# Kernel tuning notes

Hardware: AMD Instinct MI355X
Metric: run time of the kernel (lower is better)

The kernel has to match this reference:

```python
import jax, jax.numpy as jnp
import numpy as np

DIM = 2048
NUM_HEADS = 16
HEAD_DIM = DIM // NUM_HEADS  # 128
B, T = 2, 2048
ROPE_BASE = 10000.0


def _rope_tables(seq_len, head_dim, dtype=jnp.float32):
    inv_freq = 1.0 / (ROPE_BASE ** (jnp.arange(0, head_dim, 2, dtype=jnp.float32) / head_dim))
    t = jnp.arange(seq_len, dtype=jnp.float32)
    freqs = jnp.einsum('i,j->ij', t, inv_freq)          # [T, head_dim/2]
    emb = jnp.concatenate([freqs, freqs], axis=-1)       # [T, head_dim]
    return jnp.cos(emb).astype(dtype), jnp.sin(emb).astype(dtype)


def _rotate_half(x):
    x1, x2 = jnp.split(x, 2, axis=-1)
    return jnp.concatenate([-x2, x1], axis=-1)


def setup_inputs() -> dict:
    key = jax.random.key(0)
    k1, k2, k3 = jax.random.split(key, 3)
    x = jax.random.normal(k1, (B, T, DIM), dtype=jnp.float32)
    w_qkv = jax.random.normal(k2, (3 * DIM, DIM), dtype=jnp.float32) * (DIM ** -0.5)
    w_out = jax.random.normal(k3, (DIM, DIM), dtype=jnp.float32) * (DIM ** -0.5)
    return {"x": x, "w_qkv": w_qkv, "w_out": w_out}


def reference(x, w_qkv, w_out):
    b, t, _ = x.shape
    scale = HEAD_DIM ** -0.5

    qkv = x @ w_qkv.T                                    # [B, T, 3*dim]
    q, k, v = jnp.split(qkv, 3, axis=-1)
    # [B, H, T, hd]
    q = q.reshape(b, t, NUM_HEADS, HEAD_DIM).transpose(0, 2, 1, 3)
    k = k.reshape(b, t, NUM_HEADS, HEAD_DIM).transpose(0, 2, 1, 3)
    v = v.reshape(b, t, NUM_HEADS, HEAD_DIM).transpose(0, 2, 1, 3)

    cos, sin = _rope_tables(t, HEAD_DIM, x.dtype)        # [T, hd] broadcast over B,H
    q = q * cos + _rotate_half(q) * sin
    k = k * cos + _rotate_half(k) * sin

    scores = jnp.einsum('bhqd,bhkd->bhqk', q, k) * scale  # [B, H, T, T]
    causal = jnp.tril(jnp.ones((t, t), dtype=bool))
    scores = jnp.where(causal, scores, jnp.float32(-jnp.inf).astype(scores.dtype))
    attn = jax.nn.softmax(scores, axis=-1)
    out = jnp.einsum('bhqk,bhkd->bhqd', attn, v)         # [B, H, T, hd]
    out = out.transpose(0, 2, 1, 3).reshape(b, t, DIM)
    out = out @ w_out.T
    return out
```

## Files before the change

kernel.cpp:

```cpp
#include <hip/hip_runtime.h>
#include <hip/hip_bf16.h>
#include <stdint.h>
#include <math.h>

#define DIMC 2048
#define NH 16
#define HD 128
#define BBATCH 2
#define TSEQ 2048
#define MROWS (BBATCH*TSEQ)
#define NQKV (3*DIMC)

typedef __attribute__((ext_vector_type(8))) short short8;
typedef __attribute__((ext_vector_type(4))) float f32x4;

__device__ __forceinline__ short f2bf(float f) {
  union { float f; uint32_t u; } v; v.f = f;
  uint32_t r = (v.u + 0x7fffu + ((v.u >> 16) & 1u)) >> 16;
  return (short)(uint16_t)r;
}
__device__ __forceinline__ float bf2f(short s) {
  union { uint32_t u; float f; } v; v.u = ((uint32_t)(uint16_t)s) << 16;
  return v.f;
}
__device__ __forceinline__ void g2lds16(const void* g, void* l) {
  __builtin_amdgcn_global_load_lds((const __attribute__((address_space(1))) void*)g,
                                   (__attribute__((address_space(3))) void*)l, 16, 0, 0);
}

__global__ void rope_tables(float* __restrict__ cos_t, float* __restrict__ sin_t) {
  int idx = blockIdx.x * blockDim.x + threadIdx.x;
  int t = idx >> 6, j = idx & 63;
  double inv = exp(-((double)(2 * j) / 128.0) * log(10000.0));
  float fr = (float)t * (float)inv;
  cos_t[idx] = cosf(fr);
  sin_t[idx] = sinf(fr);
}

__global__ void cast_f32_bf16(const float* __restrict__ in, short* __restrict__ out, int n8) {
  int i = blockIdx.x * blockDim.x + threadIdx.x;
  if (i >= n8) return;
  const float4* p = (const float4*)in;
  float4 a = p[2 * i], b = p[2 * i + 1];
  short8 o;
  o[0] = f2bf(a.x); o[1] = f2bf(a.y); o[2] = f2bf(a.z); o[3] = f2bf(a.w);
  o[4] = f2bf(b.x); o[5] = f2bf(b.y); o[6] = f2bf(b.z); o[7] = f2bf(b.w);
  ((short8*)out)[i] = o;
}

__global__ void rope_apply(short* __restrict__ q, short* __restrict__ k,
                           const float* __restrict__ cos_t, const float* __restrict__ sin_t) {
  int idx = blockIdx.x * blockDim.x + threadIdx.x;
  int j = idx & 63;
  int t = (idx >> 6) & (TSEQ - 1);
  int bh = idx >> 17;
  size_t base = ((size_t)bh * TSEQ + t) * HD;
  float c = cos_t[t * 64 + j], s = sin_t[t * 64 + j];
  float x1 = bf2f(q[base + j]), x2 = bf2f(q[base + j + 64]);
  q[base + j]      = f2bf(x1 * c - x2 * s);
  q[base + j + 64] = f2bf(x2 * c + x1 * s);
  float y1 = bf2f(k[base + j]), y2 = bf2f(k[base + j + 64]);
  k[base + j]      = f2bf(y1 * c - y2 * s);
  k[base + j + 64] = f2bf(y2 * c + y1 * s);
}

template<int EPI>
__global__ __launch_bounds__(256)
void gemm_bt(const short* __restrict__ A, const short* __restrict__ B,
             int M, int N, int K,
             float* __restrict__ Cout,
             short* __restrict__ qp, short* __restrict__ kp, short* __restrict__ vp) {
  __shared__ short As[128 * 32];
  __shared__ short Bs[128 * 32];
  int tid = threadIdx.x;
  int lane = tid & 63, wave = tid >> 6;
  int wr = wave >> 1, wc = wave & 1;
  int bm = blockIdx.y, bn = blockIdx.x;
  int rowA0 = bm * 128, rowB0 = bn * 128;
  f32x4 acc[4][4] = {};
  for (int k0 = 0; k0 < K; k0 += 32) {
    #pragma unroll
    for (int j = 0; j < 2; ++j) {
      int c = tid + j * 256;
      int r = c >> 2, kk = (c & 3) * 8;
      g2lds16(A + (size_t)(rowA0 + r) * K + k0 + kk, As + c * 8);
      g2lds16(B + (size_t)(rowB0 + r) * K + k0 + kk, Bs + c * 8);
    }
    __syncthreads();
    short8 af[4], bfr[4];
    #pragma unroll
    for (int mf = 0; mf < 4; ++mf)
      af[mf] = *(const short8*)(As + (wr * 64 + mf * 16 + (lane & 15)) * 32 + 8 * (lane >> 4));
    #pragma unroll
    for (int nf = 0; nf < 4; ++nf)
      bfr[nf] = *(const short8*)(Bs + (wc * 64 + nf * 16 + (lane & 15)) * 32 + 8 * (lane >> 4));
    #pragma unroll
    for (int mf = 0; mf < 4; ++mf)
      #pragma unroll
      for (int nf = 0; nf < 4; ++nf)
        acc[mf][nf] = __builtin_amdgcn_mfma_f32_16x16x32_bf16(af[mf], bfr[nf], acc[mf][nf], 0, 0, 0);
    __syncthreads();
  }
  if (EPI == 1) {
    #pragma unroll
    for (int mf = 0; mf < 4; ++mf)
      #pragma unroll
      for (int nf = 0; nf < 4; ++nf)
        #pragma unroll
        for (int i = 0; i < 4; ++i) {
          int gm = rowA0 + wr * 64 + mf * 16 + ((lane >> 4) << 2) + i;
          int gn = rowB0 + wc * 64 + nf * 16 + (lane & 15);
          Cout[(size_t)gm * N + gn] = acc[mf][nf][i];
        }
  } else {
    short* dst = (bn < 16) ? qp : (bn < 32) ? kp : vp;
    int h = bn & 15;
    #pragma unroll
    for (int mf = 0; mf < 4; ++mf)
      #pragma unroll
      for (int nf = 0; nf < 4; ++nf)
        #pragma unroll
        for (int i = 0; i < 4; ++i) {
          int gm = rowA0 + wr * 64 + mf * 16 + ((lane >> 4) << 2) + i;
          int b = gm >> 11, t = gm & 2047;
          int d = wc * 64 + nf * 16 + (lane & 15);
          dst[(((size_t)b * NH + h) * TSEQ + t) * HD + d] = f2bf(acc[mf][nf][i]);
        }
  }
}

__global__ __launch_bounds__(256)
void flash_attn(const short* __restrict__ Q, const short* __restrict__ K,
                const short* __restrict__ V, short* __restrict__ Oout) {
  __shared__ short Ks[64 * 128];
  __shared__ short Vt[128 * 64];
  __shared__ short Pl[4 * 16 * 64];
  int tid = threadIdx.x, lane = tid & 63, wave = tid >> 6;
  int bid = blockIdx.x;
  int qt = (TSEQ / 64 - 1) - (bid >> 5);
  int hb = bid & 31;
  int h = hb & 15, b = hb >> 4;
  size_t bh_off = ((size_t)b * NH + h) * TSEQ * HD;
  const short* Qp = Q + bh_off;
  const short* Kp = K + bh_off;
  const short* Vp = V + bh_off;
  int q0 = qt * 64 + wave * 16;
  short8 qf[4];
  #pragma unroll
  for (int ks = 0; ks < 4; ++ks)
    qf[ks] = *(const short8*)(Qp + (size_t)(q0 + (lane & 15)) * HD + ks * 32 + 8 * (lane >> 4));
  float m_run[4], l_run[4];
  f32x4 acc_o[8] = {};
  #pragma unroll
  for (int i = 0; i < 4; ++i) { m_run[i] = -INFINITY; l_run[i] = 0.f; }
  const float scale = 0.08838834764831845f;
  for (int it = 0; it <= qt; ++it) {
    int kv0 = it * 64;
    short8 vv[4];
    #pragma unroll
    for (int j = 0; j < 4; ++j) {
      int e = tid + j * 256;
      int r = e >> 4, c0 = (e & 15) * 8;
      vv[j] = *(const short8*)(Vp + (size_t)(kv0 + r) * HD + c0);
    }
    #pragma unroll
    for (int j = 0; j < 4; ++j) {
      int c = tid + j * 256;
      int r = c >> 4, cc = c & 15;
      g2lds16(Kp + (size_t)(kv0 + r) * HD + ((cc ^ (r & 7)) << 3), Ks + c * 8);
    }
    #pragma unroll
    for (int j = 0; j < 4; ++j) {
      int e = tid + j * 256;
      int r = e >> 4, c0 = (e & 15) * 8;
      int rc = r >> 3, rl = r & 7;
      #pragma unroll
      for (int jj = 0; jj < 8; ++jj) {
        int d = c0 + jj;
        int pch = rc ^ (d & 7) ^ ((d >> 3) & 7);
        Vt[d * 64 + (pch << 3) + rl] = vv[j][jj];
      }
    }
    __syncthreads();
    f32x4 sa[4] = {};
    __builtin_amdgcn_s_setprio(1);
    #pragma unroll
    for (int nf = 0; nf < 4; ++nf)
      #pragma unroll
      for (int ks = 0; ks < 4; ++ks) {
        int row = nf * 16 + (lane & 15);
        int lch = ks * 4 + (lane >> 4);
        short8 kf = *(const short8*)(Ks + row * 128 + ((lch ^ (row & 7)) << 3));
        sa[nf] = __builtin_amdgcn_mfma_f32_16x16x32_bf16(qf[ks], kf, sa[nf], 0, 0, 0);
      }
    __builtin_amdgcn_s_setprio(0);
    bool lastTile = (it == qt);
    #pragma unroll
    for (int nf = 0; nf < 4; ++nf)
      #pragma unroll
      for (int i = 0; i < 4; ++i) {
        float s = sa[nf][i] * scale;
        if (lastTile) {
          int kvc = kv0 + nf * 16 + (lane & 15);
          int qr = q0 + ((lane >> 4) << 2) + i;
          if (kvc > qr) s = -INFINITY;
        }
        sa[nf][i] = s;
      }
    #pragma unroll
    for (int i = 0; i < 4; ++i) {
      float t = fmaxf(fmaxf(sa[0][i], sa[1][i]), fmaxf(sa[2][i], sa[3][i]));
      t = fmaxf(t, __shfl_xor(t, 1));
      t = fmaxf(t, __shfl_xor(t, 2));
      t = fmaxf(t, __shfl_xor(t, 4));
      t = fmaxf(t, __shfl_xor(t, 8));
      float mn = fmaxf(m_run[i], t);
      float al = __expf(m_run[i] - mn);
      m_run[i] = mn;
      float su = 0.f;
      #pragma unroll
      for (int nf = 0; nf < 4; ++nf) {
        float p = __expf(sa[nf][i] - mn);
        sa[nf][i] = p;
        su += p;
      }
      su += __shfl_xor(su, 1);
      su += __shfl_xor(su, 2);
      su += __shfl_xor(su, 4);
      su += __shfl_xor(su, 8);
      l_run[i] = l_run[i] * al + su;
      #pragma unroll
      for (int nfd = 0; nfd < 8; ++nfd) acc_o[nfd][i] *= al;
    }
    short* Pw = Pl + wave * 16 * 64;
    #pragma unroll
    for (int nf = 0; nf < 4; ++nf)
      #pragma unroll
      for (int i = 0; i < 4; ++i) {
        int qq = ((lane >> 4) << 2) + i;
        int kv = nf * 16 + (lane & 15);
        Pw[qq * 64 + (((kv >> 3) ^ (qq & 7)) << 3) + (kv & 7)] = f2bf(sa[nf][i]);
      }
    __builtin_amdgcn_s_setprio(1);
    #pragma unroll
    for (int ks2 = 0; ks2 < 2; ++ks2) {
      int qq = lane & 15;
      int lchp = ks2 * 4 + (lane >> 4);
      short8 pf = *(const short8*)(Pw + qq * 64 + ((lchp ^ (qq & 7)) << 3));
      #pragma unroll
      for (int nfd = 0; nfd < 8; ++nfd) {
        int d = nfd * 16 + (lane & 15);
        int lch = ks2 * 4 + (lane >> 4);
        int pch = lch ^ (d & 7) ^ ((d >> 3) & 7);
        short8 vf = *(const short8*)(Vt + d * 64 + (pch << 3));
        acc_o[nfd] = __builtin_amdgcn_mfma_f32_16x16x32_bf16(pf, vf, acc_o[nfd], 0, 0, 0);
      }
    }
    __builtin_amdgcn_s_setprio(0);
    __syncthreads();
  }
  #pragma unroll
  for (int nfd = 0; nfd < 8; ++nfd)
    #pragma unroll
    for (int i = 0; i < 4; ++i) {
      int qr = q0 + ((lane >> 4) << 2) + i;
      int col = h * HD + nfd * 16 + (lane & 15);
      Oout[((size_t)b * TSEQ + qr) * DIMC + col] = f2bf(acc_o[nfd][i] / l_run[i]);
    }
}

extern "C" void kernel_launch(void* const* d_in, const int* in_sizes, int n_in,
                              void* d_out, int out_size, void* d_ws, size_t ws_size,
                              hipStream_t stream) {
  const float* x     = (const float*)d_in[0];
  const float* w_qkv = (const float*)d_in[1];
  const float* w_out = (const float*)d_in[2];
  float* out = (float*)d_out;
  char* ws = (char*)d_ws;
  size_t off = 0;
  auto alloc = [&](size_t bytes) {
    void* p = ws + off;
    off += (bytes + 255) & ~(size_t)255;
    return p;
  };
  float* cos_t = (float*)alloc((size_t)TSEQ * 64 * 4);
  float* sin_t = (float*)alloc((size_t)TSEQ * 64 * 4);
  short* xb    = (short*)alloc((size_t)MROWS * DIMC * 2);
  short* wqkvb = (short*)alloc((size_t)NQKV * DIMC * 2);
  short* woutb = (short*)alloc((size_t)DIMC * DIMC * 2);
  short* q     = (short*)alloc((size_t)BBATCH * NH * TSEQ * HD * 2);
  short* k     = (short*)alloc((size_t)BBATCH * NH * TSEQ * HD * 2);
  short* v     = (short*)alloc((size_t)BBATCH * NH * TSEQ * HD * 2);
  short* attn  = (short*)alloc((size_t)MROWS * DIMC * 2);

  rope_tables<<<(TSEQ * 64) / 256, 256, 0, stream>>>(cos_t, sin_t);
  cast_f32_bf16<<<(MROWS * DIMC / 8 + 255) / 256, 256, 0, stream>>>(x, xb, MROWS * DIMC / 8);
  cast_f32_bf16<<<(NQKV * DIMC / 8 + 255) / 256, 256, 0, stream>>>(w_qkv, wqkvb, NQKV * DIMC / 8);
  cast_f32_bf16<<<(DIMC * DIMC / 8 + 255) / 256, 256, 0, stream>>>(w_out, woutb, DIMC * DIMC / 8);

  gemm_bt<0><<<dim3(NQKV / 128, MROWS / 128), 256, 0, stream>>>(
      xb, wqkvb, MROWS, NQKV, DIMC, nullptr, q, k, v);

  rope_apply<<<(BBATCH * NH * TSEQ * 64) / 256, 256, 0, stream>>>(q, k, cos_t, sin_t);

  flash_attn<<<dim3((TSEQ / 64) * NH * BBATCH), 256, 0, stream>>>(q, k, v, attn);

  gemm_bt<1><<<dim3(DIMC / 128, MROWS / 128), 256, 0, stream>>>(
      attn, woutb, MROWS, DIMC, DIMC, out, nullptr, nullptr, nullptr);
}
```

Measured before the change: 438.6 us.

## Rewrite GEMMs as 256x128 tiles with multi-buffered async LDS pipeline and swizzle

New measurement: 447.1 us. About the same (+1.9%).

```diff
diff --git a/kernel.cpp b/kernel.cpp
--- a/kernel.cpp
+++ b/kernel.cpp
@@ -13,6 +13,8 @@
 
 typedef __attribute__((ext_vector_type(8))) short short8;
 typedef __attribute__((ext_vector_type(4))) float f32x4;
+
+#define BAR() asm volatile("s_barrier" ::: "memory")
 
 __device__ __forceinline__ short f2bf(float f) {
   union { float f; uint32_t u; } v; v.f = f;
@@ -64,67 +66,111 @@
   k[base + j + 64] = f2bf(y2 * c + y1 * s);
 }
 
+__device__ __forceinline__ void stage128(short* lds_base, const short* gsrc, int ldg, int tid) {
+  #pragma unroll
+  for (int j = 0; j < 2; ++j) {
+    int L = j * 512 + tid;
+    int r = L >> 3, pc = L & 7;
+    g2lds16(gsrc + (size_t)r * ldg + ((pc ^ (r & 7)) << 3), lds_base + L * 8);
+  }
+}
+__device__ __forceinline__ short8 ldsfrag(const short* base, int row, int c) {
+  return *(const short8*)(base + row * 64 + ((c ^ (row & 7)) << 3));
+}
+
 template<int EPI>
-__global__ __launch_bounds__(256)
-void gemm_bt(const short* __restrict__ A, const short* __restrict__ B,
+__global__ __launch_bounds__(512, 2)
+void gemm256(const short* __restrict__ A, const short* __restrict__ B,
              int M, int N, int K,
              float* __restrict__ Cout,
              short* __restrict__ qp, short* __restrict__ kp, short* __restrict__ vp) {
-  __shared__ short As[128 * 32];
-  __shared__ short Bs[128 * 32];
-  int tid = threadIdx.x;
-  int lane = tid & 63, wave = tid >> 6;
-  int wr = wave >> 1, wc = wave & 1;
-  int bm = blockIdx.y, bn = blockIdx.x;
-  int rowA0 = bm * 128, rowB0 = bn * 128;
-  f32x4 acc[4][4] = {};
-  for (int k0 = 0; k0 < K; k0 += 32) {
-    #pragma unroll
-    for (int j = 0; j < 2; ++j) {
-      int c = tid + j * 256;
-      int r = c >> 2, kk = (c & 3) * 8;
-      g2lds16(A + (size_t)(rowA0 + r) * K + k0 + kk, As + c * 8);
-      g2lds16(B + (size_t)(rowB0 + r) * K + k0 + kk, Bs + c * 8);
-    }
-    __syncthreads();
-    short8 af[4], bfr[4];
-    #pragma unroll
-    for (int mf = 0; mf < 4; ++mf)
-      af[mf] = *(const short8*)(As + (wr * 64 + mf * 16 + (lane & 15)) * 32 + 8 * (lane >> 4));
-    #pragma unroll
-    for (int nf = 0; nf < 4; ++nf)
-      bfr[nf] = *(const short8*)(Bs + (wc * 64 + nf * 16 + (lane & 15)) * 32 + 8 * (lane >> 4));
-    #pragma unroll
-    for (int mf = 0; mf < 4; ++mf)
-      #pragma unroll
-      for (int nf = 0; nf < 4; ++nf)
-        acc[mf][nf] = __builtin_amdgcn_mfma_f32_16x16x32_bf16(af[mf], bfr[nf], acc[mf][nf], 0, 0, 0);
-    __syncthreads();
+  __shared__ short Ab[2][256 * 64];
+  __shared__ short Bb[3][128 * 64];
+  const int tid = threadIdx.x;
+  const int lane = tid & 63, wave = tid >> 6;
+  const int wm = wave >> 2, wn = wave & 3;
+  const int bn = blockIdx.x, bm = blockIdx.y;
+  const int rowA0 = bm * 256, rowB0 = bn * 128;
+  const int NT = K / 64;
+  const int l15 = lane & 15, l4 = lane >> 4;
+  f32x4 acc[8][2] = {};
+
+  stage128(&Ab[0][0],        A + (size_t)rowA0 * K,         K, tid);
+  stage128(&Ab[0][128 * 64], A + (size_t)(rowA0 + 128) * K, K, tid);
+  stage128(&Bb[0][0],        B + (size_t)rowB0 * K,         K, tid);
+  stage128(&Bb[1][0],        B + (size_t)rowB0 * K + 64,    K, tid);
+  asm volatile("s_waitcnt vmcnt(2)" ::: "memory");
+  BAR();
+
+  for (int t = 0; t < NT; ++t) {
+    const short* At = Ab[t & 1];
+    const short* Bt = Bb[t % 3];
+    short* Anx = Ab[(t + 1) & 1];
+    short* Bnx = Bb[(t + 2) % 3];
+    const short* Ag = A + (size_t)rowA0 * K + (t + 1) * 64;
+    const short* Bg = B + (size_t)rowB0 * K + (t + 2) * 64;
+    short8 bfrag[2][2];
+    #pragma unroll
+    for (int ph = 0; ph < 4; ++ph) {
+      short8 afrag[2][2];
+      if (ph == 0) {
+        #pragma unroll
+        for (int n = 0; n < 2; ++n)
+          #pragma unroll
+          for (int ks = 0; ks < 2; ++ks)
+            bfrag[n][ks] = ldsfrag(Bt, wn * 32 + n * 16 + l15, ks * 4 + l4);
+      }
+      #pragma unroll
+      for (int m2 = 0; m2 < 2; ++m2)
+        #pragma unroll
+        for (int ks = 0; ks < 2; ++ks)
+          afrag[m2][ks] = ldsfrag(At, wm * 128 + (ph * 2 + m2) * 16 + l15, ks * 4 + l4);
+      if (ph == 0 && t + 1 < NT) stage128(Anx,            Ag,                    K, tid);
+      if (ph == 1 && t + 1 < NT) stage128(Anx + 128 * 64, Ag + (size_t)128 * K,  K, tid);
+      if (ph == 2 && t + 2 < NT) stage128(Bnx,            Bg,                    K, tid);
+      if (ph == 3) {
+        if (t + 2 < NT) asm volatile("s_waitcnt vmcnt(2)" ::: "memory");
+        else            asm volatile("s_waitcnt vmcnt(0)" ::: "memory");
+      }
+      BAR();
+      __builtin_amdgcn_s_setprio(1);
+      #pragma unroll
+      for (int m2 = 0; m2 < 2; ++m2)
+        #pragma unroll
+        for (int n = 0; n < 2; ++n)
+          #pragma unroll
+          for (int ks = 0; ks < 2; ++ks)
+            acc[ph * 2 + m2][n] =
+                __builtin_amdgcn_mfma_f32_16x16x32_bf16(afrag[m2][ks], bfrag[n][ks],
+                                                        acc[ph * 2 + m2][n], 0, 0, 0);
+      __builtin_amdgcn_s_setprio(0);
+    }
   }
+
   if (EPI == 1) {
     #pragma unroll
-    for (int mf = 0; mf < 4; ++mf)
-      #pragma unroll
-      for (int nf = 0; nf < 4; ++nf)
+    for (int m = 0; m < 8; ++m)
+      #pragma unroll
+      for (int n = 0; n < 2; ++n)
         #pragma unroll
         for (int i = 0; i < 4; ++i) {
-          int gm = rowA0 + wr * 64 + mf * 16 + ((lane >> 4) << 2) + i;
-          int gn = rowB0 + wc * 64 + nf * 16 + (lane & 15);
-          Cout[(size_t)gm * N + gn] = acc[mf][nf][i];
+          int gm = rowA0 + wm * 128 + m * 16 + (l4 << 2) + i;
+          int gn = rowB0 + wn * 32 + n * 16 + l15;
+          Cout[(size_t)gm * N + gn] = acc[m][n][i];
         }
   } else {
     short* dst = (bn < 16) ? qp : (bn < 32) ? kp : vp;
     int h = bn & 15;
     #pragma unroll
-    for (int mf = 0; mf < 4; ++mf)
-      #pragma unroll
-      for (int nf = 0; nf < 4; ++nf)
+    for (int m = 0; m < 8; ++m)
+      #pragma unroll
+      for (int n = 0; n < 2; ++n)
         #pragma unroll
         for (int i = 0; i < 4; ++i) {
-          int gm = rowA0 + wr * 64 + mf * 16 + ((lane >> 4) << 2) + i;
-          int b = gm >> 11, t = gm & 2047;
-          int d = wc * 64 + nf * 16 + (lane & 15);
-          dst[(((size_t)b * NH + h) * TSEQ + t) * HD + d] = f2bf(acc[mf][nf][i]);
+          int gm = rowA0 + wm * 128 + m * 16 + (l4 << 2) + i;
+          int b = gm >> 11, tt = gm & 2047;
+          int d = wn * 32 + n * 16 + l15;
+          dst[(((size_t)b * NH + h) * TSEQ + tt) * HD + d] = f2bf(acc[m][n][i]);
         }
   }
 }
@@ -298,13 +344,13 @@
   cast_f32_bf16<<<(NQKV * DIMC / 8 + 255) / 256, 256, 0, stream>>>(w_qkv, wqkvb, NQKV * DIMC / 8);
   cast_f32_bf16<<<(DIMC * DIMC / 8 + 255) / 256, 256, 0, stream>>>(w_out, woutb, DIMC * DIMC / 8);
 
-  gemm_bt<0><<<dim3(NQKV / 128, MROWS / 128), 256, 0, stream>>>(
+  gemm256<0><<<dim3(NQKV / 128, MROWS / 256), 512, 0, stream>>>(
       xb, wqkvb, MROWS, NQKV, DIMC, nullptr, q, k, v);
 
   rope_apply<<<(BBATCH * NH * TSEQ * 64) / 256, 256, 0, stream>>>(q, k, cos_t, sin_t);
 
   flash_attn<<<dim3((TSEQ / 64) * NH * BBATCH), 256, 0, stream>>>(q, k, v, attn);
 
-  gemm_bt<1><<<dim3(DIMC / 128, MROWS / 128), 256, 0, stream>>>(
+  gemm256<1><<<dim3(DIMC / 128, MROWS / 256), 512, 0, stream>>>(
       attn, woutb, MROWS, DIMC, DIMC, out, nullptr, nullptr, nullptr);
 }
```
